# Optimization experiments

Measured on AMD Instinct MI355X. Metric: run time of the kernel, lower is better.

The kernel has to match this reference:

```python
import jax, jax.numpy as jnp
import numpy as np

OUT_H, OUT_W = 64, 64  # glimpse size (layer's output_dim)
B, IMG_H, IMG_W, CH = 32, 512, 512, 3


def setup_inputs() -> dict:
    key = jax.random.key(0)
    k_img, k_u, k_s, k_d, k_u2, k_s2, k_d2 = jax.random.split(key, 7)
    img_tensor = jax.random.uniform(k_img, (B, IMG_H, IMG_W, CH), dtype=jnp.float32)
    # DRAW-style params per sample: (uy, sy, dy, ux, sx, dx)
    # centres u in [0, img - glimpse], sigma s in [1, 5], stride d in [1, img/glimpse]
    uy = jax.random.uniform(k_u, (B, 1), minval=0.0, maxval=IMG_H - OUT_H * 2.0)
    sy = jax.random.uniform(k_s, (B, 1), minval=1.0, maxval=5.0)
    dy = jax.random.uniform(k_d, (B, 1), minval=1.0, maxval=IMG_H / OUT_H)
    ux = jax.random.uniform(k_u2, (B, 1), minval=0.0, maxval=IMG_W - OUT_W * 2.0)
    sx = jax.random.uniform(k_s2, (B, 1), minval=1.0, maxval=5.0)
    dx = jax.random.uniform(k_d2, (B, 1), minval=1.0, maxval=IMG_W / OUT_W)
    transform_params = jnp.concatenate([uy, sy, dy, ux, sx, dx], axis=-1)  # (B, 6)
    return {"img_tensor": img_tensor, "transform_params": transform_params}


def gaussian_mask(u, s, d, R, C):
    """Normalized Gaussian filterbank.
    u, s, d: (B, 1) centre of first Gaussian, std, stride between centres.
    R: number of glimpse rows/cols; C: image size along that axis.
    Returns (B, C, R), each column normalized to sum 1 (plus eps)."""
    r = jnp.arange(R, dtype=jnp.float32).reshape(1, 1, R)
    c = jnp.arange(C, dtype=jnp.float32).reshape(1, C, 1)
    centres = u[:, None, :] + r * d[:, None, :]            # (B, 1, R)
    mask = jnp.exp(-0.5 * jnp.square((c - centres) / s[:, None, :]))  # (B, C, R)
    return mask / (jnp.sum(mask, axis=1, keepdims=True) + 1e-8)


def reference(img_tensor, transform_params):
    # img_tensor: (B, h, w, ch); transform_params: (B, 6)
    _, h, w, _ = img_tensor.shape
    uy, sy, dy, ux, sx, dx = jnp.split(transform_params, 6, axis=-1)
    Ay = gaussian_mask(uy, sy, dy, OUT_H, h)  # (B, h, OUT_H)
    Ax = gaussian_mask(ux, sx, dx, OUT_W, w)  # (B, w, OUT_W)
    # glimpse = Ay^T @ img @ Ax, applied per channel
    g = jnp.einsum('bhH,bhwc->bHwc', Ay, img_tensor)   # (B, OUT_H, w, ch)
    return jnp.einsum('bHwc,bwW->bHWc', g, Ax)         # (B, OUT_H, OUT_W, ch)
```

## Files before the change

### kernel.cpp

```cpp
#include <hip/hip_runtime.h>
#include <stdint.h>

#define BATCH 32
#define IMG 512
#define CH 3
#define GOUT 64
#define ROWB (IMG*CH)
#define GP   ((size_t)BATCH*CH*GOUT*IMG)

typedef __attribute__((ext_vector_type(8))) short  short8;
typedef __attribute__((ext_vector_type(4))) float  floatx4;
typedef __attribute__((ext_vector_type(4))) float  floatv4;

__device__ __forceinline__ unsigned short f2bf(float x) {
    unsigned u = __builtin_bit_cast(unsigned, x);
    u += 0x7FFFu + ((u >> 16) & 1u);
    return (unsigned short)(u >> 16);
}

typedef __attribute__((address_space(3))) unsigned int  lds_u32;
typedef __attribute__((address_space(1))) const unsigned int g_u32;
__device__ __forceinline__ void async16(const void* g, void* l) {
    __builtin_amdgcn_global_load_lds((g_u32*)(uintptr_t)g,
                                     (lds_u32*)(uintptr_t)l, 16, 0, 0);
}

__global__ __launch_bounds__(64) void mask_kernel(const float* __restrict__ tp,
                                                  unsigned short* __restrict__ AyT,
                                                  unsigned short* __restrict__ AxT) {
    int blk  = blockIdx.x;
    int r    = blk & 63;
    int axis = (blk >> 6) & 1;
    int b    = blk >> 7;

    const float* p = tp + b*6 + (axis ? 3 : 0);
    float u = p[0], s = p[1], d = p[2];
    float centre = u + (float)r * d;
    float inv_s  = 1.0f / s;

    int lane = threadIdx.x;
    float e[8];
    float sum = 0.0f;
    #pragma unroll
    for (int i = 0; i < 8; ++i) {
        float z = ((float)(i*64 + lane) - centre) * inv_s;
        e[i] = __expf(-0.5f * z * z);
        sum += e[i];
    }
    #pragma unroll
    for (int m = 1; m < 64; m <<= 1)
        sum += __shfl_xor(sum, m, 64);
    float inv_sum = 1.0f / (sum + 1e-8f);

    unsigned short* dst = (axis ? AxT : AyT) + ((size_t)b*GOUT + r) * IMG;
    #pragma unroll
    for (int i = 0; i < 8; ++i)
        dst[i*64 + lane] = f2bf(e[i] * inv_sum);
}

__global__ __launch_bounds__(256, 2) void stage1_kernel(const float* __restrict__ img,
                                                        const unsigned short* __restrict__ AyT,
                                                        float* __restrict__ gP) {
    __shared__ float Bs[256][64];

    int part = blockIdx.x & 1;
    int bt   = blockIdx.x >> 1;
    int tile = bt % 24;
    int b    = bt / 24;
    int wc0  = tile * 64;
    int tid  = threadIdx.x;
    int wave = tid >> 6;
    int lane = tid & 63;
    int n16  = lane & 15;
    int q    = lane >> 4;

    const float*          imb = img + (size_t)b * IMG * ROWB + wc0;
    const unsigned short* ayb = AyT + (size_t)b * GOUT * IMG;
    int h0 = part * 256;

    #pragma unroll
    for (int i = 0; i < 16; ++i) {
        int r = wave*64 + i*4 + q;
        async16(imb + (size_t)(h0 + r) * ROWB + n16*4, &Bs[r][n16*4]);
    }

    floatx4 acc[4];
    #pragma unroll
    for (int mt = 0; mt < 4; ++mt) acc[mt] = (floatx4){0.f, 0.f, 0.f, 0.f};

    __syncthreads();

    #pragma unroll
    for (int kk = 0; kk < 8; ++kk) {
        short8 bf;
        #pragma unroll
        for (int j = 0; j < 8; ++j)
            bf[j] = (short)f2bf(Bs[kk*32 + q*8 + j][wave*16 + n16]);
        int hk = h0 + kk*32 + q*8;
        #pragma unroll
        for (int mt = 0; mt < 4; ++mt) {
            short8 af = *(const short8*)(ayb + (size_t)(mt*16 + n16) * IMG + hk);
            acc[mt] = __builtin_amdgcn_mfma_f32_16x16x32_bf16(af, bf, acc[mt], 0, 0, 0);
        }
    }

    int wc = wc0 + wave*16 + n16;
    int c = wc % 3, w = wc / 3;
    float* gb = gP + (size_t)part * GP + ((size_t)(b*CH + c) * GOUT) * IMG + w;
    #pragma unroll
    for (int mt = 0; mt < 4; ++mt)
        #pragma unroll
        for (int reg = 0; reg < 4; ++reg)
            gb[(size_t)(mt*16 + q*4 + reg) * IMG] = acc[mt][reg];
}

__global__ __launch_bounds__(256, 4) void stage2_kernel(const float* __restrict__ gP,
                                                        const unsigned short* __restrict__ AxT,
                                                        float* __restrict__ out) {
    int blk  = blockIdx.x;
    int part = blk & 1;
    int hq   = (blk >> 1) & 3;
    int bc   = blk >> 3;
    int c    = bc % 3;
    int b    = bc / 3;
    int tid  = threadIdx.x;
    int wq   = tid >> 6;
    int lane = tid & 63;
    int n16  = lane & 15;
    int q    = lane >> 4;

    floatx4 acc = (floatx4){0.f, 0.f, 0.f, 0.f};

    const float*          ga  = gP  + ((size_t)(b*CH + c) * GOUT + hq*16 + n16) * IMG;
    const unsigned short* axb = AxT + ((size_t)b*GOUT + wq*16 + n16) * IMG;

    #pragma unroll
    for (int ph = 0; ph < 2; ++ph) {
        floatv4 A0[4], A1[4], B0[4], B1[4];
        short8  BF[4];
        #pragma unroll
        for (int cc = 0; cc < 4; ++cc) {
            int w0 = part*256 + ph*128 + cc*32 + q*8;
            A0[cc] = *(const floatv4*)(ga + w0);
            A1[cc] = *(const floatv4*)(ga + w0 + 4);
            B0[cc] = *(const floatv4*)(ga + GP + w0);
            B1[cc] = *(const floatv4*)(ga + GP + w0 + 4);
            BF[cc] = *(const short8*)(axb + w0);
        }
        #pragma unroll
        for (int cc = 0; cc < 4; ++cc) {
            short8 af;
            af[0] = (short)f2bf(A0[cc][0] + B0[cc][0]);
            af[1] = (short)f2bf(A0[cc][1] + B0[cc][1]);
            af[2] = (short)f2bf(A0[cc][2] + B0[cc][2]);
            af[3] = (short)f2bf(A0[cc][3] + B0[cc][3]);
            af[4] = (short)f2bf(A1[cc][0] + B1[cc][0]);
            af[5] = (short)f2bf(A1[cc][1] + B1[cc][1]);
            af[6] = (short)f2bf(A1[cc][2] + B1[cc][2]);
            af[7] = (short)f2bf(A1[cc][3] + B1[cc][3]);
            acc = __builtin_amdgcn_mfma_f32_16x16x32_bf16(af, BF[cc], acc, 0, 0, 0);
        }
    }

    float* ob = out + (((size_t)b*GOUT + hq*16) * GOUT + wq*16 + n16) * CH + c;
    #pragma unroll
    for (int reg = 0; reg < 4; ++reg)
        atomicAdd(ob + (size_t)(q*4 + reg) * GOUT * CH, acc[reg]);
}

extern "C" void kernel_launch(void* const* d_in, const int* in_sizes, int n_in,
                              void* d_out, int out_size, void* d_ws, size_t ws_size,
                              hipStream_t stream) {
    const float* img = (const float*)d_in[0];
    const float* tp  = (const float*)d_in[1];
    float* out = (float*)d_out;

    unsigned short* AyT = (unsigned short*)d_ws;
    unsigned short* AxT = AyT + (size_t)BATCH * GOUT * IMG;
    float*          gPp = (float*)(AxT + (size_t)BATCH * GOUT * IMG);

    hipMemsetAsync(d_out, 0, (size_t)out_size * sizeof(float), stream);
    mask_kernel  <<<BATCH * 2 * GOUT,    64, 0, stream>>>(tp, AyT, AxT);
    stage1_kernel<<<BATCH * 24 * 2,     256, 0, stream>>>(img, AyT, gPp);
    stage2_kernel<<<BATCH * CH * 4 * 2, 256, 0, stream>>>(gPp, AxT, out);
}
```

Baseline: 197.1 us.

## Pre-transpose image to bf16 and drop split-K partials in stage1

Adds a transpose kernel that converts the image to a bf16, column-major (per w*c, contiguous over h) layout, so stage1 can load MFMA B fragments directly from global memory instead of staging fp32 tiles in LDS and converting them. Stage1 now covers the full K=512 in one block, which removes the two-partial gP buffer and the extra partial-sum reads in stage2. The cost is an extra full pass over the image (an fp32 read plus a bf16 write and reread), an extra kernel launch, and fewer stage1 blocks with a longer serial K loop.

```diff
diff --git a/kernel.cpp b/kernel.cpp
--- a/kernel.cpp
+++ b/kernel.cpp
@@ -8,21 +8,15 @@
 #define ROWB (IMG*CH)
 #define GP   ((size_t)BATCH*CH*GOUT*IMG)
 
-typedef __attribute__((ext_vector_type(8))) short  short8;
-typedef __attribute__((ext_vector_type(4))) float  floatx4;
-typedef __attribute__((ext_vector_type(4))) float  floatv4;
+typedef __attribute__((ext_vector_type(8))) short          short8;
+typedef __attribute__((ext_vector_type(8))) unsigned short ushort8;
+typedef __attribute__((ext_vector_type(4))) float          floatx4;
+typedef __attribute__((ext_vector_type(4))) float          floatv4;
 
 __device__ __forceinline__ unsigned short f2bf(float x) {
     unsigned u = __builtin_bit_cast(unsigned, x);
     u += 0x7FFFu + ((u >> 16) & 1u);
     return (unsigned short)(u >> 16);
-}
-
-typedef __attribute__((address_space(3))) unsigned int  lds_u32;
-typedef __attribute__((address_space(1))) const unsigned int g_u32;
-__device__ __forceinline__ void async16(const void* g, void* l) {
-    __builtin_amdgcn_global_load_lds((g_u32*)(uintptr_t)g,
-                                     (lds_u32*)(uintptr_t)l, 16, 0, 0);
 }
 
 __global__ __launch_bounds__(64) void mask_kernel(const float* __restrict__ tp,
@@ -58,15 +52,42 @@
         dst[i*64 + lane] = f2bf(e[i] * inv_sum);
 }
 
-__global__ __launch_bounds__(256, 2) void stage1_kernel(const float* __restrict__ img,
+__global__ __launch_bounds__(256) void transpose_kernel(const float* __restrict__ img,
+                                                        unsigned short* __restrict__ imgT) {
+    __shared__ float Ls[32][256];
+
+    int blk = blockIdx.x;
+    int wt  = blk % 6;
+    int hs  = (blk / 6) % 16;
+    int b   = blk / 96;
+    int h0  = hs * 32;
+    int wc0 = wt * 256;
+    int t   = threadIdx.x;
+
+    const float* src = img + ((size_t)(b*IMG + h0 + (t >> 6)) * ROWB + wc0 + (t & 63)*4);
+    #pragma unroll
+    for (int rnd = 0; rnd < 8; ++rnd) {
+        floatv4 v = *(const floatv4*)(src + (size_t)rnd*4*ROWB);
+        *(floatv4*)&Ls[rnd*4 + (t >> 6)][(t & 63)*4] = v;
+    }
+    __syncthreads();
+
+    unsigned short* dst = imgT + ((size_t)(b*ROWB + wc0 + t)) * IMG + h0;
+    #pragma unroll
+    for (int seg = 0; seg < 4; ++seg) {
+        ushort8 o;
+        #pragma unroll
+        for (int j = 0; j < 8; ++j)
+            o[j] = f2bf(Ls[seg*8 + j][t]);
+        *(ushort8*)(dst + seg*8) = o;
+    }
+}
+
+__global__ __launch_bounds__(256, 4) void stage1_kernel(const unsigned short* __restrict__ imgT,
                                                         const unsigned short* __restrict__ AyT,
                                                         float* __restrict__ gP) {
-    __shared__ float Bs[256][64];
-
-    int part = blockIdx.x & 1;
-    int bt   = blockIdx.x >> 1;
-    int tile = bt % 24;
-    int b    = bt / 24;
+    int tile = blockIdx.x % 24;
+    int b    = blockIdx.x / 24;
     int wc0  = tile * 64;
     int tid  = threadIdx.x;
     int wave = tid >> 6;
@@ -74,29 +95,17 @@
     int n16  = lane & 15;
     int q    = lane >> 4;
 
-    const float*          imb = img + (size_t)b * IMG * ROWB + wc0;
-    const unsigned short* ayb = AyT + (size_t)b * GOUT * IMG;
-    int h0 = part * 256;
-
-    #pragma unroll
-    for (int i = 0; i < 16; ++i) {
-        int r = wave*64 + i*4 + q;
-        async16(imb + (size_t)(h0 + r) * ROWB + n16*4, &Bs[r][n16*4]);
-    }
-
     floatx4 acc[4];
     #pragma unroll
     for (int mt = 0; mt < 4; ++mt) acc[mt] = (floatx4){0.f, 0.f, 0.f, 0.f};
 
-    __syncthreads();
+    const unsigned short* imt = imgT + ((size_t)b*ROWB + wc0 + wave*16 + n16) * IMG;
+    const unsigned short* ayb = AyT + (size_t)b * GOUT * IMG;
 
-    #pragma unroll
-    for (int kk = 0; kk < 8; ++kk) {
-        short8 bf;
-        #pragma unroll
-        for (int j = 0; j < 8; ++j)
-            bf[j] = (short)f2bf(Bs[kk*32 + q*8 + j][wave*16 + n16]);
-        int hk = h0 + kk*32 + q*8;
+    #pragma unroll 4
+    for (int kk = 0; kk < 16; ++kk) {
+        int hk = kk*32 + q*8;
+        short8 bf = *(const short8*)(imt + hk);
         #pragma unroll
         for (int mt = 0; mt < 4; ++mt) {
             short8 af = *(const short8*)(ayb + (size_t)(mt*16 + n16) * IMG + hk);
@@ -106,7 +115,7 @@
 
     int wc = wc0 + wave*16 + n16;
     int c = wc % 3, w = wc / 3;
-    float* gb = gP + (size_t)part * GP + ((size_t)(b*CH + c) * GOUT) * IMG + w;
+    float* gb = gP + ((size_t)(b*CH + c) * GOUT) * IMG + w;
     #pragma unroll
     for (int mt = 0; mt < 4; ++mt)
         #pragma unroll
@@ -136,28 +145,26 @@
 
     #pragma unroll
     for (int ph = 0; ph < 2; ++ph) {
-        floatv4 A0[4], A1[4], B0[4], B1[4];
+        floatv4 A0[4], A1[4];
         short8  BF[4];
         #pragma unroll
         for (int cc = 0; cc < 4; ++cc) {
             int w0 = part*256 + ph*128 + cc*32 + q*8;
             A0[cc] = *(const floatv4*)(ga + w0);
             A1[cc] = *(const floatv4*)(ga + w0 + 4);
-            B0[cc] = *(const floatv4*)(ga + GP + w0);
-            B1[cc] = *(const floatv4*)(ga + GP + w0 + 4);
             BF[cc] = *(const short8*)(axb + w0);
         }
         #pragma unroll
         for (int cc = 0; cc < 4; ++cc) {
             short8 af;
-            af[0] = (short)f2bf(A0[cc][0] + B0[cc][0]);
-            af[1] = (short)f2bf(A0[cc][1] + B0[cc][1]);
-            af[2] = (short)f2bf(A0[cc][2] + B0[cc][2]);
-            af[3] = (short)f2bf(A0[cc][3] + B0[cc][3]);
-            af[4] = (short)f2bf(A1[cc][0] + B1[cc][0]);
-            af[5] = (short)f2bf(A1[cc][1] + B1[cc][1]);
-            af[6] = (short)f2bf(A1[cc][2] + B1[cc][2]);
-            af[7] = (short)f2bf(A1[cc][3] + B1[cc][3]);
+            af[0] = (short)f2bf(A0[cc][0]);
+            af[1] = (short)f2bf(A0[cc][1]);
+            af[2] = (short)f2bf(A0[cc][2]);
+            af[3] = (short)f2bf(A0[cc][3]);
+            af[4] = (short)f2bf(A1[cc][0]);
+            af[5] = (short)f2bf(A1[cc][1]);
+            af[6] = (short)f2bf(A1[cc][2]);
+            af[7] = (short)f2bf(A1[cc][3]);
             acc = __builtin_amdgcn_mfma_f32_16x16x32_bf16(af, BF[cc], acc, 0, 0, 0);
         }
     }
@@ -175,12 +182,14 @@
     const float* tp  = (const float*)d_in[1];
     float* out = (float*)d_out;
 
-    unsigned short* AyT = (unsigned short*)d_ws;
-    unsigned short* AxT = AyT + (size_t)BATCH * GOUT * IMG;
-    float*          gPp = (float*)(AxT + (size_t)BATCH * GOUT * IMG);
+    unsigned short* AyT  = (unsigned short*)d_ws;
+    unsigned short* AxT  = AyT + (size_t)BATCH * GOUT * IMG;
+    unsigned short* imgT = AxT + (size_t)BATCH * GOUT * IMG;
+    float*          gPp  = (float*)(imgT + (size_t)BATCH * ROWB * IMG);
 
     hipMemsetAsync(d_out, 0, (size_t)out_size * sizeof(float), stream);
-    mask_kernel  <<<BATCH * 2 * GOUT,    64, 0, stream>>>(tp, AyT, AxT);
-    stage1_kernel<<<BATCH * 24 * 2,     256, 0, stream>>>(img, AyT, gPp);
-    stage2_kernel<<<BATCH * CH * 4 * 2, 256, 0, stream>>>(gPp, AxT, out);
+    transpose_kernel<<<BATCH * 16 * 6,     256, 0, stream>>>(img, imgT);
+    mask_kernel     <<<BATCH * 2 * GOUT,    64, 0, stream>>>(tp, AyT, AxT);
+    stage1_kernel   <<<BATCH * 24,         256, 0, stream>>>(imgT, AyT, gPp);
+    stage2_kernel   <<<BATCH * CH * 4 * 2, 256, 0, stream>>>(gPp, AxT, out);
 }
```

New measurement: 212.1 us. +7.6%, slower.
